# Performance work log

Measured on AMD Instinct MI355X. Metric: run time of the kernel, lower is better.

## Reference

```python
import jax, jax.numpy as jnp
import numpy as np

B, L, E, H = 4, 1024, 2048, 16
DH = E // H
SCALE_BASE = 512.0


def _rotate_every_two(x):
    x1 = x[..., ::2]
    x2 = x[..., 1::2]
    return jnp.stack([-x2, x1], axis=-1).reshape(x.shape)


def _xpos(x, downscale):
    # x: [BH, L, Dh]; non-incremental path => offset = 0
    length = x.shape[1]
    head_dim = x.shape[-1]
    min_pos = -(length // 2)
    positions = jnp.arange(min_pos, length + min_pos, dtype=jnp.float32)  # [L]
    base = (jnp.arange(0, head_dim, 2, dtype=jnp.float32) + 0.4 * head_dim) / (1.4 * head_dim)  # [Dh/2]
    scale = base[None, :] ** (positions[:, None] / SCALE_BASE)  # [L, Dh/2]
    # fixed_pos_embedding over `scale` (seq_len=L, dim=Dh/2), positions 0..L-1
    dim = head_dim // 2
    inv_freq = 1.0 / (10000.0 ** (jnp.arange(0, dim, dtype=jnp.float32) / dim))
    sinusoid = jnp.arange(length, dtype=jnp.float32)[:, None] * inv_freq[None, :]
    sin, cos = jnp.sin(sinusoid), jnp.cos(sinusoid)
    if downscale:
        scale = 1.0 / scale
    sin_s = jnp.repeat(sin * scale, 2, axis=-1)  # duplicate_interleave -> [L, Dh]
    cos_s = jnp.repeat(cos * scale, 2, axis=-1)
    return x * cos_s + _rotate_every_two(x) * sin_s


def setup_inputs() -> dict:
    key = jax.random.key(0)
    ks = jax.random.split(key, 6)
    w_std = 1.0 / np.sqrt(E)
    query = jax.random.normal(ks[0], (B, L, E), dtype=jnp.float32)
    Wq = jax.random.normal(ks[1], (E, E), dtype=jnp.float32) * w_std
    Wk = jax.random.normal(ks[2], (E, E), dtype=jnp.float32) * w_std
    Wv = jax.random.normal(ks[3], (E, E), dtype=jnp.float32) * w_std
    Wo = jax.random.normal(ks[4], (E, E), dtype=jnp.float32) * w_std
    bq = jnp.zeros((E,), jnp.float32)
    bk = jnp.zeros((E,), jnp.float32)
    bv = jnp.zeros((E,), jnp.float32)
    bo = jnp.zeros((E,), jnp.float32)
    # causal additive mask [L, L]: 0 on/below diag, large negative above
    attn_mask = jnp.where(jnp.triu(jnp.ones((L, L), bool), k=1), -1e9, 0.0).astype(jnp.float32)
    rel_pos = jax.random.normal(ks[5], (B * H, L, L), dtype=jnp.float32) * 0.02
    return {"query": query, "Wq": Wq, "bq": bq, "Wk": Wk, "bk": bk, "Wv": Wv,
            "bv": bv, "Wo": Wo, "bo": bo, "attn_mask": attn_mask, "rel_pos": rel_pos}


def reference(query, Wq, bq, Wk, bk, Wv, bv, Wo, bo, attn_mask, rel_pos):
    scaling = DH ** -0.5
    q = (query @ Wq.T + bq) * scaling
    k = query @ Wk.T + bk
    v = query @ Wv.T + bv

    def split(t):  # [B, L, E] -> [B*H, L, Dh]
        return t.reshape(B, L, H, DH).transpose(0, 2, 1, 3).reshape(B * H, L, DH)

    q, k, v = split(q), split(k), split(v)
    k = _xpos(k, downscale=True)
    q = _xpos(q, downscale=False)

    w = jnp.einsum('btd,bsd->bts', q, k)          # [B*H, L, L]
    w = jnp.nan_to_num(w) + attn_mask[None]
    w = w + rel_pos
    w = jax.nn.softmax(w.astype(jnp.float32), axis=-1).astype(w.dtype)
    attn = jnp.einsum('bts,bsd->btd', w, v)       # [B*H, L, Dh]
    attn = attn.reshape(B, H, L, DH).transpose(0, 2, 1, 3).reshape(B, L, E)
    out = attn @ Wo.T + bo
    attn_weights = w.reshape(B, H, L, L).transpose(1, 0, 2, 3)  # [H, B, L, L]
    return out, attn_weights
```

## Files before the change

kernel.cpp:

```cpp
#include <hip/hip_runtime.h>
#include <math.h>

#define BB 4
#define LL 1024
#define EE 2048
#define HH 16
#define DHD 128
#define NTOK 4096
#define NBH 64
#define OUT0_ELEMS 8388608

typedef __attribute__((ext_vector_type(8))) short short8;
typedef __attribute__((ext_vector_type(4))) float f32x4;
typedef __attribute__((ext_vector_type(4))) unsigned short ushort4v;
typedef __attribute__((ext_vector_type(8))) unsigned short ushort8v;

__device__ __forceinline__ unsigned short f2bf(float x) {
    union { float f; unsigned int u; } v; v.f = x;
    unsigned int r = v.u + 0x7FFFu + ((v.u >> 16) & 1u);
    return (unsigned short)(r >> 16);
}
__device__ __forceinline__ float bf2f(unsigned short h) {
    union { unsigned int u; float f; } v; v.u = ((unsigned int)h) << 16;
    return v.f;
}

__device__ __forceinline__ void gload16(const void* g, void* l) {
    __builtin_amdgcn_global_load_lds((const __attribute__((address_space(1))) void*)g,
                                     (__attribute__((address_space(3))) void*)l,
                                     16, 0, 0);
}

__global__ __launch_bounds__(256)
void cvt_all_k(const float* __restrict__ X, const float* __restrict__ Wq,
               const float* __restrict__ Wk, const float* __restrict__ Wv,
               const float* __restrict__ Wo, unsigned short* __restrict__ Xbf,
               unsigned short* __restrict__ Wqkvb, unsigned short* __restrict__ Wob) {
    size_t g = (size_t)(blockIdx.x * 256 + threadIdx.x) * 8;
    if (g >= 25165824u) return;
    const float* src;
    unsigned short* dst;
    if (g < 8388608u) {
        src = X + g; dst = Xbf + g;
    } else {
        size_t rr = g - 8388608u;
        int wi = (int)(rr >> 22);
        size_t o = rr & 4194303u;
        src = (wi == 0 ? Wq : wi == 1 ? Wk : wi == 2 ? Wv : Wo) + o;
        dst = (wi < 3 ? Wqkvb + ((size_t)wi << 22) : Wob) + o;
    }
    float4 a = *(const float4*)(src);
    float4 b = *(const float4*)(src + 4);
    ushort4v u, w;
    u.x = f2bf(a.x); u.y = f2bf(a.y); u.z = f2bf(a.z); u.w = f2bf(a.w);
    w.x = f2bf(b.x); w.y = f2bf(b.y); w.z = f2bf(b.z); w.w = f2bf(b.w);
    *(ushort4v*)(dst) = u;
    *(ushort4v*)(dst + 4) = w;
}

__global__ __launch_bounds__(64) void xpos_table_k(float4* __restrict__ tab) {
    int t = blockIdx.x;
    int j = threadIdx.x;
    float pos = (float)(t - 512);
    float base = (2.0f * (float)j + 51.2f) * (1.0f / 179.2f);
    float sc = powf(base, pos * (1.0f / 512.0f));
    float inv_freq = powf(10000.0f, -(float)j * (1.0f / 64.0f));
    float ang = (float)t * inv_freq;
    float s = sinf(ang);
    float c = cosf(ang);
    tab[(t << 6) | j] = make_float4(c * sc, s * sc, c / sc, s / sc);
}

template <int MODE>
__global__ __launch_bounds__(512, 2)
void mm8_k(const unsigned short* __restrict__ Abf, const unsigned short* __restrict__ Bw,
           const float* __restrict__ bq, const float* __restrict__ bk,
           const float* __restrict__ bv, unsigned short* __restrict__ qb,
           unsigned short* __restrict__ kb, unsigned short* __restrict__ vt,
           const float4* __restrict__ tab, float* __restrict__ Cout,
           float scaling) {
    __shared__ alignas(16) char smem[98304];

    const int tid = threadIdx.x;
    const int lane = tid & 63;
    const int wid = tid >> 6;
    const int wr = wid >> 2;
    const int wcn = wid & 3;
    const int fr = lane & 15, fq = lane >> 4;

    const int m0 = blockIdx.y * 128, n0 = blockIdx.x * 256;

    auto stageA = [&](int T) {
        char* dst = smem + ((T & 1) << 14);
        const unsigned short* src = Abf + (size_t)m0 * 2048 + T * 64;
#pragma unroll
        for (int j = 0; j < 2; ++j) {
            int o = (j * 512 + tid) * 16;
            int r = o >> 7;
            int cs = ((o & 127) >> 4) ^ (r & 7);
            gload16(src + (size_t)r * 2048 + cs * 8, dst + o);
        }
    };
    auto stageB = [&](int T, int half) {
        char* dst = smem + 32768 + ((T & 1) << 15) + (half << 14);
        const unsigned short* src = Bw + (size_t)(n0 + half * 128) * 2048 + T * 64;
#pragma unroll
        for (int j = 0; j < 2; ++j) {
            int o = (j * 512 + tid) * 16;
            int r = o >> 7;
            int cs = ((o & 127) >> 4) ^ (r & 7);
            gload16(src + (size_t)r * 2048 + cs * 8, dst + o);
        }
    };
    auto rdA = [&](int buf, int mi, int ks) -> short8 {
        int rl = (wr << 6) + mi * 16 + fr;
        const char* base = smem + (buf << 14);
        return *(const short8*)(base + rl * 128 + ((ks * 4 + fq) ^ (rl & 7)) * 16);
    };
    auto rdB = [&](int buf, int ni, int ks) -> short8 {
        int rb = wcn * 64 + ni * 16 + fr;
        const char* base = smem + 32768 + (buf << 15) + ((rb >> 7) << 14);
        int rh = rb & 127;
        return *(const short8*)(base + rh * 128 + ((ks * 4 + fq) ^ (rh & 7)) * 16);
    };

    f32x4 acc[4][4];
#pragma unroll
    for (int i = 0; i < 4; ++i)
#pragma unroll
        for (int j = 0; j < 4; ++j) acc[i][j] = (f32x4){0.f, 0.f, 0.f, 0.f};

    stageA(0); stageB(0, 0); stageB(0, 1); stageB(1, 0); stageB(1, 1);

    for (int T = 0; T < 32; ++T) {
        const int buf = T & 1;
        if (T < 31) asm volatile("s_waitcnt vmcnt(4)" ::: "memory");
        else        asm volatile("s_waitcnt vmcnt(0)" ::: "memory");
        __builtin_amdgcn_s_barrier();

        short8 a0[2][2], a1[2][2], b0[2][2], b1[2][2];

#pragma unroll
        for (int mi = 0; mi < 2; ++mi) { a0[mi][0] = rdA(buf, mi, 0); a0[mi][1] = rdA(buf, mi, 1); }
#pragma unroll
        for (int ni = 0; ni < 2; ++ni) { b0[ni][0] = rdB(buf, ni, 0); b0[ni][1] = rdB(buf, ni, 1); }
        if (T < 31) stageA(T + 1);
        __builtin_amdgcn_s_barrier();
        __builtin_amdgcn_s_setprio(1);
#pragma unroll
        for (int mi = 0; mi < 2; ++mi)
#pragma unroll
            for (int ni = 0; ni < 2; ++ni) {
                acc[mi][ni] = __builtin_amdgcn_mfma_f32_16x16x32_bf16(a0[mi][0], b0[ni][0], acc[mi][ni], 0, 0, 0);
                acc[mi][ni] = __builtin_amdgcn_mfma_f32_16x16x32_bf16(a0[mi][1], b0[ni][1], acc[mi][ni], 0, 0, 0);
            }
        __builtin_amdgcn_s_setprio(0);
        __builtin_amdgcn_s_barrier();

#pragma unroll
        for (int ni = 0; ni < 2; ++ni) { b1[ni][0] = rdB(buf, ni + 2, 0); b1[ni][1] = rdB(buf, ni + 2, 1); }
        __builtin_amdgcn_s_barrier();
        __builtin_amdgcn_s_setprio(1);
#pragma unroll
        for (int mi = 0; mi < 2; ++mi)
#pragma unroll
            for (int ni = 0; ni < 2; ++ni) {
                acc[mi][ni + 2] = __builtin_amdgcn_mfma_f32_16x16x32_bf16(a0[mi][0], b1[ni][0], acc[mi][ni + 2], 0, 0, 0);
                acc[mi][ni + 2] = __builtin_amdgcn_mfma_f32_16x16x32_bf16(a0[mi][1], b1[ni][1], acc[mi][ni + 2], 0, 0, 0);
            }
        __builtin_amdgcn_s_setprio(0);
        __builtin_amdgcn_s_barrier();

#pragma unroll
        for (int mi = 0; mi < 2; ++mi) { a1[mi][0] = rdA(buf, mi + 2, 0); a1[mi][1] = rdA(buf, mi + 2, 1); }
        if (T < 30) stageB(T + 2, 0);
        __builtin_amdgcn_s_barrier();
        __builtin_amdgcn_s_setprio(1);
#pragma unroll
        for (int mi = 0; mi < 2; ++mi)
#pragma unroll
            for (int ni = 0; ni < 2; ++ni) {
                acc[mi + 2][ni] = __builtin_amdgcn_mfma_f32_16x16x32_bf16(a1[mi][0], b0[ni][0], acc[mi + 2][ni], 0, 0, 0);
                acc[mi + 2][ni] = __builtin_amdgcn_mfma_f32_16x16x32_bf16(a1[mi][1], b0[ni][1], acc[mi + 2][ni], 0, 0, 0);
            }
        __builtin_amdgcn_s_setprio(0);
        __builtin_amdgcn_s_barrier();

        if (T < 30) stageB(T + 2, 1);
        __builtin_amdgcn_s_barrier();
        __builtin_amdgcn_s_setprio(1);
#pragma unroll
        for (int mi = 0; mi < 2; ++mi)
#pragma unroll
            for (int ni = 0; ni < 2; ++ni) {
                acc[mi + 2][ni + 2] = __builtin_amdgcn_mfma_f32_16x16x32_bf16(a1[mi][0], b1[ni][0], acc[mi + 2][ni + 2], 0, 0, 0);
                acc[mi + 2][ni + 2] = __builtin_amdgcn_mfma_f32_16x16x32_bf16(a1[mi][1], b1[ni][1], acc[mi + 2][ni + 2], 0, 0, 0);
            }
        __builtin_amdgcn_s_setprio(0);
        __builtin_amdgcn_s_barrier();
    }

    if constexpr (MODE == 1) {
        const float* bias = bq;
#pragma unroll
        for (int mi = 0; mi < 4; ++mi)
#pragma unroll
            for (int ni = 0; ni < 4; ++ni)
#pragma unroll
                for (int rg = 0; rg < 4; ++rg) {
                    int m = m0 + wr * 64 + mi * 16 + fq * 4 + rg;
                    int n = n0 + wcn * 64 + ni * 16 + fr;
                    Cout[(size_t)m * EE + n] = acc[mi][ni][rg] + bias[n];
                }
        return;
    } else {
        const int w = n0 >> 11;
        const float* bsel = (w == 0) ? bq : (w == 1) ? bk : bv;
        const float alpha = (w == 0) ? scaling : 1.0f;
        const int hbase = (n0 & 2047) >> 7;
        const int b_ = m0 >> 10;
        const int m0r = m0 & 1023;
        float* slab = (float*)smem;

        unsigned short* qk = (w == 0) ? qb : kb;
        __syncthreads();
#pragma unroll
        for (int sl = 0; sl < 4; ++sl) {
            if (wr == (sl >> 1)) {
#pragma unroll
                for (int mi2 = 0; mi2 < 2; ++mi2) {
                    int mi = ((sl & 1) << 1) + mi2;
#pragma unroll
                    for (int ni = 0; ni < 4; ++ni) {
                        int scol = wcn * 64 + ni * 16 + fr;
                        float bias = bsel[(n0 & 2047) + scol];
#pragma unroll
                        for (int rg = 0; rg < 4; ++rg) {
                            int srow = (mi2 << 4) + fq * 4 + rg;
                            slab[srow * 260 + scol] = alpha * (acc[mi][ni][rg] + bias);
                        }
                    }
                }
            }
            __syncthreads();

            if (w < 2) {
                int sr = tid >> 4, cg = tid & 15;
                int t = m0r + (sl << 5) + sr;
                int h = hbase + (cg >> 3);
                int d0 = (cg & 7) << 4;
                const float* SR = slab + sr * 260 + cg * 16;
                ushort8v h0, h1;
#pragma unroll
                for (int p = 0; p < 4; ++p) {
                    float x = SR[2 * p], y = SR[2 * p + 1];
                    float4 tb = tab[(t << 6) | ((d0 >> 1) + p)];
                    float c = (w == 0) ? tb.x : tb.z;
                    float s = (w == 0) ? tb.y : tb.w;
                    h0[2 * p]     = f2bf(x * c - y * s);
                    h0[2 * p + 1] = f2bf(y * c + x * s);
                }
#pragma unroll
                for (int p = 0; p < 4; ++p) {
                    float x = SR[8 + 2 * p], y = SR[8 + 2 * p + 1];
                    float4 tb = tab[(t << 6) | ((d0 >> 1) + 4 + p)];
                    float c = (w == 0) ? tb.x : tb.z;
                    float s = (w == 0) ? tb.y : tb.w;
                    h1[2 * p]     = f2bf(x * c - y * s);
                    h1[2 * p + 1] = f2bf(y * c + x * s);
                }
                unsigned short* DR = qk + (((size_t)(b_ * HH + h)) << 17) + ((size_t)t << 7) + d0;
                *(ushort8v*)(DR) = h0;
                *(ushort8v*)(DR + 8) = h1;
            } else {
                int vcol = tid >> 1, th = tid & 1;
                int h = hbase + (vcol >> 7), d = vcol & 127;
                ushort8v h0, h1;
#pragma unroll
                for (int p = 0; p < 8; ++p)
                    h0[p] = f2bf(slab[(th * 16 + p) * 260 + vcol]);
#pragma unroll
                for (int p = 0; p < 8; ++p)
                    h1[p] = f2bf(slab[(th * 16 + 8 + p) * 260 + vcol]);
                unsigned short* DR = vt + (((size_t)((b_ * HH + h) * 128 + d)) << 10)
                                     + m0r + (sl << 5) + th * 16;
                *(ushort8v*)(DR) = h0;
                *(ushort8v*)(DR + 8) = h1;
            }
            __syncthreads();
        }
    }
}

__global__ __launch_bounds__(256)
void scores_k(const unsigned short* __restrict__ qb, const unsigned short* __restrict__ kb,
              const float* __restrict__ rel, unsigned short* __restrict__ ebuf,
              float* __restrict__ psum) {
    __shared__ alignas(16) char smem[16384];
    unsigned short* lA = (unsigned short*)smem;
    unsigned short* lB = (unsigned short*)(smem + 8192);
    float* slab = (float*)smem;

    const int tid = threadIdx.x;
    const int lane = tid & 63, wave = tid >> 6;
    const int wr = wave >> 1, wc = wave & 1;
    const int fr = lane & 15, fq = lane >> 4;

    const int flat = blockIdx.y * 36 + blockIdx.x;
    const int xcd = flat & 7, rmp = flat >> 3;
    int idx = rmp % 36;
    const int bh = (rmp / 36) * 8 + xcd;

    int tt = (int)((sqrtf(8.f * (float)idx + 1.f) - 1.f) * 0.5f);
    while ((tt + 1) * (tt + 2) / 2 <= idx) ++tt;
    while (tt * (tt + 1) / 2 > idx) --tt;
    const int ss = idx - tt * (tt + 1) / 2;
    const int t0 = tt << 7, s0 = ss << 7;

    const unsigned short* Q = qb + ((size_t)bh << 17);
    const unsigned short* K = kb + ((size_t)bh << 17);

    f32x4 acc[4][4];
#pragma unroll
    for (int i = 0; i < 4; ++i)
#pragma unroll
        for (int j = 0; j < 4; ++j) acc[i][j] = (f32x4){0.f, 0.f, 0.f, 0.f};

    for (int k0 = 0; k0 < 128; k0 += 32) {
#pragma unroll
        for (int i = 0; i < 2; ++i) {
            int c = i * 256 + tid;
            int r = c >> 2, kc = c & 3;
            gload16(Q + (size_t)(t0 + r) * 128 + k0 + kc * 8, &lA[c * 8]);
        }
#pragma unroll
        for (int i = 0; i < 2; ++i) {
            int c = i * 256 + tid;
            int r = c >> 2, kc = c & 3;
            gload16(K + (size_t)(s0 + r) * 128 + k0 + kc * 8, &lB[c * 8]);
        }
        __syncthreads();

        short8 afr[4], bfr[4];
#pragma unroll
        for (int mi = 0; mi < 4; ++mi)
            afr[mi] = *(const short8*)&lA[(wr * 64 + mi * 16 + fr) * 32 + fq * 8];
#pragma unroll
        for (int ni = 0; ni < 4; ++ni)
            bfr[ni] = *(const short8*)&lB[(wc * 64 + ni * 16 + fr) * 32 + fq * 8];
#pragma unroll
        for (int mi = 0; mi < 4; ++mi)
#pragma unroll
            for (int ni = 0; ni < 4; ++ni)
                acc[mi][ni] = __builtin_amdgcn_mfma_f32_16x16x32_bf16(
                    afr[mi], bfr[ni], acc[mi][ni], 0, 0, 0);
        __syncthreads();
    }

    unsigned short* EO = ebuf + ((size_t)bh << 20);
    const float* RLb = rel + ((size_t)bh << 20);
#pragma unroll
    for (int sl = 0; sl < 4; ++sl) {
        if (wr == (sl >> 1)) {
#pragma unroll
            for (int mi2 = 0; mi2 < 2; ++mi2) {
                int mi = ((sl & 1) << 1) + mi2;
#pragma unroll
                for (int ni = 0; ni < 4; ++ni)
#pragma unroll
                    for (int r = 0; r < 4; ++r) {
                        int srow = (mi2 << 4) + (fq << 2) + r;
                        int col = (wc << 6) + (ni << 4) + fr;
                        slab[srow * 128 + (col ^ (((srow >> 2) & 3) << 4))] = acc[mi][ni][r];
                    }
            }
        }
        __syncthreads();
        {
            int srow = tid >> 3;
            int tg = t0 + (sl << 5) + srow;
            const float* RL = RLb + ((size_t)tg << 10) + s0;
            unsigned short* ER = EO + ((size_t)tg << 10) + s0;
            float rsum = 0.f;
#pragma unroll
            for (int c = 0; c < 4; ++c) {
                int col = ((tid & 7) << 2) + (c << 5);
                float4 sv = *(const float4*)&slab[srow * 128 + (col ^ (((srow >> 2) & 3) << 4))];
                float4 rl = *(const float4*)(RL + col);
                float4 e;
                e.x = (s0 + col     <= tg) ? __expf(sv.x + rl.x - 15.f) : 0.f;
                e.y = (s0 + col + 1 <= tg) ? __expf(sv.y + rl.y - 15.f) : 0.f;
                e.z = (s0 + col + 2 <= tg) ? __expf(sv.z + rl.z - 15.f) : 0.f;
                e.w = (s0 + col + 3 <= tg) ? __expf(sv.w + rl.w - 15.f) : 0.f;
                ushort4v h;
                h.x = f2bf(e.x); h.y = f2bf(e.y); h.z = f2bf(e.z); h.w = f2bf(e.w);
                *(ushort4v*)(ER + col) = h;
                rsum += e.x + e.y + e.z + e.w;
            }
            rsum += __shfl_xor(rsum, 1);
            rsum += __shfl_xor(rsum, 2);
            rsum += __shfl_xor(rsum, 4);
            if ((tid & 7) == 0)
                psum[((((size_t)bh << 10) + tg) << 3) + ss] = rsum;
        }
        __syncthreads();
    }
}

__global__ __launch_bounds__(256)
void pvw_k(const unsigned short* __restrict__ ebuf, const unsigned short* __restrict__ vt,
           const float* __restrict__ psum, float* __restrict__ attnP,
           unsigned short* __restrict__ am) {
    __shared__ alignas(16) unsigned short lE[64 * 64];
    __shared__ alignas(16) unsigned short lV[128 * 64];
    __shared__ float lInvF[64];

    const int tid = threadIdx.x;
    const int lane = tid & 63, wave = tid >> 6;
    const int wr = wave >> 1, wc = wave & 1;
    const int fr = lane & 15, fq = lane >> 4;
    const int strip = 15 - blockIdx.y;
    const int t0 = strip << 6;
    const int bh = blockIdx.x;
    const int hh = bh & 15, bb = bh >> 4;
    const int n_s = (t0 >> 6) + 1;

    const unsigned short* EB = ebuf + ((size_t)bh << 20) + ((size_t)t0 << 10);
    const unsigned short* Vb = vt + ((size_t)bh << 17);
    float* PO = attnP + (((size_t)(hh * BB + bb)) << 20) + ((size_t)t0 << 10);

    if (tid < 64) {
        const float* p = psum + ((((size_t)bh << 10) + t0 + tid) << 3);
        const int tt = t0 >> 7;
        float s = 0.f;
#pragma unroll
        for (int j = 0; j < 8; ++j) s += (j <= tt) ? p[j] : 0.f;
        lInvF[tid] = 1.f / s;
    }
    __syncthreads();

    f32x4 acc[2][4];
#pragma unroll
    for (int i = 0; i < 2; ++i)
#pragma unroll
        for (int j = 0; j < 4; ++j) acc[i][j] = (f32x4){0.f, 0.f, 0.f, 0.f};

    for (int j = 0; j < n_s; ++j) {
        int s0 = j << 6;
#pragma unroll
        for (int i = 0; i < 2; ++i) {
            int o = (i * 256 + tid) * 16;
            int r = o >> 7;
            int cb = (o & 127) ^ ((r & 7) << 4);
            gload16(EB + (size_t)r * 1024 + s0 + (cb >> 1), (char*)lE + o);
        }
#pragma unroll
        for (int i = 0; i < 4; ++i) {
            int o = (i * 256 + tid) * 16;
            int r = o >> 7;
            int cb = (o & 127) ^ ((r & 7) << 4);
            gload16(Vb + (size_t)r * 1024 + s0 + (cb >> 1), (char*)lV + o);
        }
        __syncthreads();

        {
            int row = tid >> 2, col0 = (tid & 3) << 4;
            float inv = lInvF[row];
            float* PR = PO + (size_t)row * 1024 + s0 + col0;
#pragma unroll
            for (int cc = 0; cc < 2; ++cc) {
                int cbyte = ((col0 + cc * 8) * 2) ^ ((row & 7) << 4);
                ushort8v ev = *(const ushort8v*)((const char*)lE + row * 128 + cbyte);
                float4 p0, p1;
                p0.x = bf2f(ev[0]) * inv; p0.y = bf2f(ev[1]) * inv;
                p0.z = bf2f(ev[2]) * inv; p0.w = bf2f(ev[3]) * inv;
                p1.x = bf2f(ev[4]) * inv; p1.y = bf2f(ev[5]) * inv;
                p1.z = bf2f(ev[6]) * inv; p1.w = bf2f(ev[7]) * inv;
                *(float4*)(PR + cc * 8) = p0;
                *(float4*)(PR + cc * 8 + 4) = p1;
            }
        }

#pragma unroll
        for (int ks = 0; ks < 2; ++ks) {
            short8 pf[2], vf[4];
#pragma unroll
            for (int mi = 0; mi < 2; ++mi) {
                int row = wr * 32 + mi * 16 + fr;
                int cb = (ks * 64 + fq * 16) ^ ((row & 7) << 4);
                pf[mi] = *(const short8*)((const char*)lE + row * 128 + cb);
            }
#pragma unroll
            for (int ni = 0; ni < 4; ++ni) {
                int row = wc * 64 + ni * 16 + fr;
                int cb = (ks * 64 + fq * 16) ^ ((row & 7) << 4);
                vf[ni] = *(const short8*)((const char*)lV + row * 128 + cb);
            }
#pragma unroll
            for (int mi = 0; mi < 2; ++mi)
#pragma unroll
                for (int ni = 0; ni < 4; ++ni)
                    acc[mi][ni] = __builtin_amdgcn_mfma_f32_16x16x32_bf16(
                        pf[mi], vf[ni], acc[mi][ni], 0, 0, 0);
        }
        __syncthreads();
    }

    {
        int row = tid >> 2;
        float4 z = make_float4(0.f, 0.f, 0.f, 0.f);
        for (int c = (n_s << 6) + ((tid & 3) << 2); c < 1024; c += 16)
            *(float4*)(PO + (size_t)row * 1024 + c) = z;
    }

#pragma unroll
    for (int mi = 0; mi < 2; ++mi)
#pragma unroll
        for (int ni = 0; ni < 4; ++ni)
#pragma unroll
            for (int r = 0; r < 4; ++r) {
                int tl = wr * 32 + mi * 16 + fq * 4 + r;
                int d = wc * 64 + ni * 16 + fr;
                float o = acc[mi][ni][r] * lInvF[tl];
                am[(((size_t)(bb * 1024 + t0 + tl)) << 11) + hh * 128 + d] = f2bf(o);
            }
}

extern "C" void kernel_launch(void* const* d_in, const int* in_sizes, int n_in,
                              void* d_out, int out_size, void* d_ws, size_t ws_size,
                              hipStream_t stream) {
    const float* query = (const float*)d_in[0];
    const float* Wq    = (const float*)d_in[1];
    const float* bq    = (const float*)d_in[2];
    const float* Wk    = (const float*)d_in[3];
    const float* bk    = (const float*)d_in[4];
    const float* Wv    = (const float*)d_in[5];
    const float* bv    = (const float*)d_in[6];
    const float* Wo    = (const float*)d_in[7];
    const float* bo    = (const float*)d_in[8];
    const float* rel   = (const float*)d_in[10];

    float* out    = (float*)d_out;
    float* attn_w = out + OUT0_ELEMS;

    char* w = (char*)d_ws;
    unsigned short* Xbf   = (unsigned short*)(w);
    unsigned short* Wqkvb = (unsigned short*)(w + (16 << 20));
    unsigned short* Wob   = (unsigned short*)(w + (40 << 20));
    unsigned short* qb    = (unsigned short*)(w + (48 << 20));
    unsigned short* kb    = (unsigned short*)(w + (64 << 20));
    unsigned short* vt    = (unsigned short*)(w + (80 << 20));
    unsigned short* am    = (unsigned short*)(w + (96 << 20));
    float4* tab           = (float4*)(w + (112 << 20));
    float* psum           = (float*)(w + (113u << 20));
    unsigned short* ebuf  = (unsigned short*)(w + (128u << 20));

    const float scaling = 0.08838834764831845f;

    xpos_table_k<<<LL, 64, 0, stream>>>(tab);

    cvt_all_k<<<12288, 256, 0, stream>>>(query, Wq, Wk, Wv, Wo, Xbf, Wqkvb, Wob);

    dim3 gqkv(24, 32);
    mm8_k<0><<<gqkv, 512, 0, stream>>>(Xbf, Wqkvb, bq, bk, bv, qb, kb, vt, tab,
                                       nullptr, scaling);

    dim3 gsc(36, NBH);
    scores_k<<<gsc, 256, 0, stream>>>(qb, kb, rel, ebuf, psum);

    dim3 gpv(NBH, 16);
    pvw_k<<<gpv, 256, 0, stream>>>(ebuf, vt, psum, attn_w, am);

    dim3 gout(8, 32);
    mm8_k<1><<<gout, 512, 0, stream>>>(am, Wob, bo, nullptr, nullptr, nullptr,
                                       nullptr, nullptr, tab, out, 1.0f);
}
```

Baseline: 426.7 us.

## Double-buffer LDS tiles in scores and PV kernels to overlap loads with MFMA

Both the QK^T scores kernel and the PV/weights kernel now keep two LDS buffers and issue the global-to-LDS loads for the next k-step or s-tile before computing the current one. Partial s_waitcnt vmcnt waits and raw s_barrier replace the full __syncthreads, so in-flight prefetches are not drained. The aim is to hide global load latency behind MFMA work. In exchange it doubles LDS use per block, which may lower occupancy, and it relies on hand-counted vmcnt values that must match the number of outstanding loads.

```diff
diff --git a/kernel.cpp b/kernel.cpp
--- a/kernel.cpp
+++ b/kernel.cpp
@@ -296,9 +296,7 @@
 void scores_k(const unsigned short* __restrict__ qb, const unsigned short* __restrict__ kb,
               const float* __restrict__ rel, unsigned short* __restrict__ ebuf,
               float* __restrict__ psum) {
-    __shared__ alignas(16) char smem[16384];
-    unsigned short* lA = (unsigned short*)smem;
-    unsigned short* lB = (unsigned short*)(smem + 8192);
+    __shared__ alignas(16) char smem[32768];
     float* slab = (float*)smem;
 
     const int tid = threadIdx.x;
@@ -320,41 +318,53 @@
     const unsigned short* Q = qb + ((size_t)bh << 17);
     const unsigned short* K = kb + ((size_t)bh << 17);
 
-    f32x4 acc[4][4];
-#pragma unroll
-    for (int i = 0; i < 4; ++i)
-#pragma unroll
-        for (int j = 0; j < 4; ++j) acc[i][j] = (f32x4){0.f, 0.f, 0.f, 0.f};
-
-    for (int k0 = 0; k0 < 128; k0 += 32) {
+    auto stage = [&](int ks) {
+        int b = ks & 1;
+        int k0 = ks << 5;
+        unsigned short* A = (unsigned short*)(smem + b * 8192);
+        unsigned short* Bm = (unsigned short*)(smem + 16384 + b * 8192);
 #pragma unroll
         for (int i = 0; i < 2; ++i) {
             int c = i * 256 + tid;
             int r = c >> 2, kc = c & 3;
-            gload16(Q + (size_t)(t0 + r) * 128 + k0 + kc * 8, &lA[c * 8]);
+            gload16(Q + (size_t)(t0 + r) * 128 + k0 + kc * 8, &A[c * 8]);
         }
 #pragma unroll
         for (int i = 0; i < 2; ++i) {
             int c = i * 256 + tid;
             int r = c >> 2, kc = c & 3;
-            gload16(K + (size_t)(s0 + r) * 128 + k0 + kc * 8, &lB[c * 8]);
-        }
-        __syncthreads();
-
+            gload16(K + (size_t)(s0 + r) * 128 + k0 + kc * 8, &Bm[c * 8]);
+        }
+    };
+
+    f32x4 acc[4][4];
+#pragma unroll
+    for (int i = 0; i < 4; ++i)
+#pragma unroll
+        for (int j = 0; j < 4; ++j) acc[i][j] = (f32x4){0.f, 0.f, 0.f, 0.f};
+
+    stage(0);
+    for (int ks = 0; ks < 4; ++ks) {
+        if (ks < 3) { stage(ks + 1); asm volatile("s_waitcnt vmcnt(4)" ::: "memory"); }
+        else        { asm volatile("s_waitcnt vmcnt(0)" ::: "memory"); }
+        __builtin_amdgcn_s_barrier();
+
+        const unsigned short* A = (const unsigned short*)(smem + (ks & 1) * 8192);
+        const unsigned short* Bm = (const unsigned short*)(smem + 16384 + (ks & 1) * 8192);
         short8 afr[4], bfr[4];
 #pragma unroll
         for (int mi = 0; mi < 4; ++mi)
-            afr[mi] = *(const short8*)&lA[(wr * 64 + mi * 16 + fr) * 32 + fq * 8];
+            afr[mi] = *(const short8*)&A[(wr * 64 + mi * 16 + fr) * 32 + fq * 8];
 #pragma unroll
         for (int ni = 0; ni < 4; ++ni)
-            bfr[ni] = *(const short8*)&lB[(wc * 64 + ni * 16 + fr) * 32 + fq * 8];
+            bfr[ni] = *(const short8*)&Bm[(wc * 64 + ni * 16 + fr) * 32 + fq * 8];
 #pragma unroll
         for (int mi = 0; mi < 4; ++mi)
 #pragma unroll
             for (int ni = 0; ni < 4; ++ni)
                 acc[mi][ni] = __builtin_amdgcn_mfma_f32_16x16x32_bf16(
                     afr[mi], bfr[ni], acc[mi][ni], 0, 0, 0);
-        __syncthreads();
+        __builtin_amdgcn_s_barrier();
     }
 
     unsigned short* EO = ebuf + ((size_t)bh << 20);
@@ -411,8 +421,8 @@
 void pvw_k(const unsigned short* __restrict__ ebuf, const unsigned short* __restrict__ vt,
            const float* __restrict__ psum, float* __restrict__ attnP,
            unsigned short* __restrict__ am) {
-    __shared__ alignas(16) unsigned short lE[64 * 64];
-    __shared__ alignas(16) unsigned short lV[128 * 64];
+    __shared__ alignas(16) unsigned short lE[2][64 * 64];
+    __shared__ alignas(16) unsigned short lV[2][128 * 64];
     __shared__ float lInvF[64];
 
     const int tid = threadIdx.x;
@@ -423,7 +433,7 @@
     const int t0 = strip << 6;
     const int bh = blockIdx.x;
     const int hh = bh & 15, bb = bh >> 4;
-    const int n_s = (t0 >> 6) + 1;
+    const int n_s = strip + 1;
 
     const unsigned short* EB = ebuf + ((size_t)bh << 20) + ((size_t)t0 << 10);
     const unsigned short* Vb = vt + ((size_t)bh << 17);
@@ -439,29 +449,38 @@
     }
     __syncthreads();
 
-    f32x4 acc[2][4];
-#pragma unroll
-    for (int i = 0; i < 2; ++i)
-#pragma unroll
-        for (int j = 0; j < 4; ++j) acc[i][j] = (f32x4){0.f, 0.f, 0.f, 0.f};
-
-    for (int j = 0; j < n_s; ++j) {
+    auto stage = [&](int j) {
+        int b = j & 1;
         int s0 = j << 6;
 #pragma unroll
         for (int i = 0; i < 2; ++i) {
             int o = (i * 256 + tid) * 16;
             int r = o >> 7;
             int cb = (o & 127) ^ ((r & 7) << 4);
-            gload16(EB + (size_t)r * 1024 + s0 + (cb >> 1), (char*)lE + o);
+            gload16(EB + (size_t)r * 1024 + s0 + (cb >> 1), (char*)lE[b] + o);
         }
 #pragma unroll
         for (int i = 0; i < 4; ++i) {
             int o = (i * 256 + tid) * 16;
             int r = o >> 7;
             int cb = (o & 127) ^ ((r & 7) << 4);
-            gload16(Vb + (size_t)r * 1024 + s0 + (cb >> 1), (char*)lV + o);
-        }
-        __syncthreads();
+            gload16(Vb + (size_t)r * 1024 + s0 + (cb >> 1), (char*)lV[b] + o);
+        }
+    };
+
+    f32x4 acc[2][4];
+#pragma unroll
+    for (int i = 0; i < 2; ++i)
+#pragma unroll
+        for (int j = 0; j < 4; ++j) acc[i][j] = (f32x4){0.f, 0.f, 0.f, 0.f};
+
+    stage(0);
+    for (int j = 0; j < n_s; ++j) {
+        const int b = j & 1;
+        if (j + 1 < n_s) { stage(j + 1); asm volatile("s_waitcnt vmcnt(6)" ::: "memory"); }
+        else             { asm volatile("s_waitcnt vmcnt(0)" ::: "memory"); }
+        __builtin_amdgcn_s_barrier();
+        const int s0 = j << 6;
 
         {
             int row = tid >> 2, col0 = (tid & 3) << 4;
@@ -470,7 +489,7 @@
 #pragma unroll
             for (int cc = 0; cc < 2; ++cc) {
                 int cbyte = ((col0 + cc * 8) * 2) ^ ((row & 7) << 4);
-                ushort8v ev = *(const ushort8v*)((const char*)lE + row * 128 + cbyte);
+                ushort8v ev = *(const ushort8v*)((const char*)lE[b] + row * 128 + cbyte);
                 float4 p0, p1;
                 p0.x = bf2f(ev[0]) * inv; p0.y = bf2f(ev[1]) * inv;
                 p0.z = bf2f(ev[2]) * inv; p0.w = bf2f(ev[3]) * inv;
@@ -488,13 +507,13 @@
             for (int mi = 0; mi < 2; ++mi) {
                 int row = wr * 32 + mi * 16 + fr;
                 int cb = (ks * 64 + fq * 16) ^ ((row & 7) << 4);
-                pf[mi] = *(const short8*)((const char*)lE + row * 128 + cb);
+                pf[mi] = *(const short8*)((const char*)lE[b] + row * 128 + cb);
             }
 #pragma unroll
             for (int ni = 0; ni < 4; ++ni) {
                 int row = wc * 64 + ni * 16 + fr;
                 int cb = (ks * 64 + fq * 16) ^ ((row & 7) << 4);
-                vf[ni] = *(const short8*)((const char*)lV + row * 128 + cb);
+                vf[ni] = *(const short8*)((const char*)lV[b] + row * 128 + cb);
             }
 #pragma unroll
             for (int mi = 0; mi < 2; ++mi)
@@ -503,7 +522,7 @@
                     acc[mi][ni] = __builtin_amdgcn_mfma_f32_16x16x32_bf16(
                         pf[mi], vf[ni], acc[mi][ni], 0, 0, 0);
         }
-        __syncthreads();
+        __builtin_amdgcn_s_barrier();
     }
 
     {
```

Result: slower. 436.7 us (+2.4%).

## Split normalized attention-weight write out of PV kernel into streaming kernel

Applied to the files above, without the earlier changes.

Removes the fp32 normalized-probability store and the zero-fill of masked columns from the PV matmul kernel, leaving it as a pure bf16 PV product. A new row-per-wave kernel re-reads the unnormalized bf16 exponentials and the partial sums, normalizes them and writes the full attention-weight matrix, including zeros. The aim is to stop the large, causally imbalanced store traffic from stalling the MFMA loop, and to let the store run as a uniform streaming pass. The cost is an extra kernel launch and a second read of the exponential buffer.

```diff
diff --git a/kernel.cpp b/kernel.cpp
--- a/kernel.cpp
+++ b/kernel.cpp
@@ -408,9 +408,8 @@
 }
 
 __global__ __launch_bounds__(256)
-void pvw_k(const unsigned short* __restrict__ ebuf, const unsigned short* __restrict__ vt,
-           const float* __restrict__ psum, float* __restrict__ attnP,
-           unsigned short* __restrict__ am) {
+void pv_k(const unsigned short* __restrict__ ebuf, const unsigned short* __restrict__ vt,
+          const float* __restrict__ psum, unsigned short* __restrict__ am) {
     __shared__ alignas(16) unsigned short lE[64 * 64];
     __shared__ alignas(16) unsigned short lV[128 * 64];
     __shared__ float lInvF[64];
@@ -423,11 +422,10 @@
     const int t0 = strip << 6;
     const int bh = blockIdx.x;
     const int hh = bh & 15, bb = bh >> 4;
-    const int n_s = (t0 >> 6) + 1;
+    const int n_s = strip + 1;
 
     const unsigned short* EB = ebuf + ((size_t)bh << 20) + ((size_t)t0 << 10);
     const unsigned short* Vb = vt + ((size_t)bh << 17);
-    float* PO = attnP + (((size_t)(hh * BB + bb)) << 20) + ((size_t)t0 << 10);
 
     if (tid < 64) {
         const float* p = psum + ((((size_t)bh << 10) + t0 + tid) << 3);
@@ -437,7 +435,6 @@
         for (int j = 0; j < 8; ++j) s += (j <= tt) ? p[j] : 0.f;
         lInvF[tid] = 1.f / s;
     }
-    __syncthreads();
 
     f32x4 acc[2][4];
 #pragma unroll
@@ -447,6 +444,7 @@
 
     for (int j = 0; j < n_s; ++j) {
         int s0 = j << 6;
+        __syncthreads();
 #pragma unroll
         for (int i = 0; i < 2; ++i) {
             int o = (i * 256 + tid) * 16;
@@ -463,24 +461,6 @@
         }
         __syncthreads();
 
-        {
-            int row = tid >> 2, col0 = (tid & 3) << 4;
-            float inv = lInvF[row];
-            float* PR = PO + (size_t)row * 1024 + s0 + col0;
-#pragma unroll
-            for (int cc = 0; cc < 2; ++cc) {
-                int cbyte = ((col0 + cc * 8) * 2) ^ ((row & 7) << 4);
-                ushort8v ev = *(const ushort8v*)((const char*)lE + row * 128 + cbyte);
-                float4 p0, p1;
-                p0.x = bf2f(ev[0]) * inv; p0.y = bf2f(ev[1]) * inv;
-                p0.z = bf2f(ev[2]) * inv; p0.w = bf2f(ev[3]) * inv;
-                p1.x = bf2f(ev[4]) * inv; p1.y = bf2f(ev[5]) * inv;
-                p1.z = bf2f(ev[6]) * inv; p1.w = bf2f(ev[7]) * inv;
-                *(float4*)(PR + cc * 8) = p0;
-                *(float4*)(PR + cc * 8 + 4) = p1;
-            }
-        }
-
 #pragma unroll
         for (int ks = 0; ks < 2; ++ks) {
             short8 pf[2], vf[4];
@@ -503,14 +483,6 @@
                     acc[mi][ni] = __builtin_amdgcn_mfma_f32_16x16x32_bf16(
                         pf[mi], vf[ni], acc[mi][ni], 0, 0, 0);
         }
-        __syncthreads();
-    }
-
-    {
-        int row = tid >> 2;
-        float4 z = make_float4(0.f, 0.f, 0.f, 0.f);
-        for (int c = (n_s << 6) + ((tid & 3) << 2); c < 1024; c += 16)
-            *(float4*)(PO + (size_t)row * 1024 + c) = z;
     }
 
 #pragma unroll
@@ -524,6 +496,51 @@
                 float o = acc[mi][ni][r] * lInvF[tl];
                 am[(((size_t)(bb * 1024 + t0 + tl)) << 11) + hh * 128 + d] = f2bf(o);
             }
+}
+
+__global__ __launch_bounds__(256)
+void normP_k(const unsigned short* __restrict__ ebuf, const float* __restrict__ psum,
+             float* __restrict__ attnP) {
+    const int gid = blockIdx.x * 4 + (threadIdx.x >> 6);
+    const int lane = threadIdx.x & 63;
+    const int bh = gid >> 10, t = gid & 1023;
+    const int hh = bh & 15, bb = bh >> 4;
+    const int tt = t >> 7;
+    const int kend = (tt + 1) << 7;
+
+    const float* p = psum + ((size_t)gid << 3);
+    float s = 0.f;
+#pragma unroll
+    for (int j = 0; j < 8; ++j) s += (j <= tt) ? p[j] : 0.f;
+    const float inv = 1.f / s;
+
+    const unsigned short* ER = ebuf + ((size_t)gid << 10);
+    float* PR = attnP + (((size_t)(hh * BB + bb)) << 20) + ((size_t)t << 10);
+    const int col = lane << 4;
+
+    if (col < kend) {
+        ushort8v e0 = *(const ushort8v*)(ER + col);
+        ushort8v e1 = *(const ushort8v*)(ER + col + 8);
+        float4 o0, o1, o2, o3;
+        o0.x = bf2f(e0[0]) * inv; o0.y = bf2f(e0[1]) * inv;
+        o0.z = bf2f(e0[2]) * inv; o0.w = bf2f(e0[3]) * inv;
+        o1.x = bf2f(e0[4]) * inv; o1.y = bf2f(e0[5]) * inv;
+        o1.z = bf2f(e0[6]) * inv; o1.w = bf2f(e0[7]) * inv;
+        o2.x = bf2f(e1[0]) * inv; o2.y = bf2f(e1[1]) * inv;
+        o2.z = bf2f(e1[2]) * inv; o2.w = bf2f(e1[3]) * inv;
+        o3.x = bf2f(e1[4]) * inv; o3.y = bf2f(e1[5]) * inv;
+        o3.z = bf2f(e1[6]) * inv; o3.w = bf2f(e1[7]) * inv;
+        *(float4*)(PR + col)      = o0;
+        *(float4*)(PR + col + 4)  = o1;
+        *(float4*)(PR + col + 8)  = o2;
+        *(float4*)(PR + col + 12) = o3;
+    } else {
+        float4 z = make_float4(0.f, 0.f, 0.f, 0.f);
+        *(float4*)(PR + col)      = z;
+        *(float4*)(PR + col + 4)  = z;
+        *(float4*)(PR + col + 8)  = z;
+        *(float4*)(PR + col + 12) = z;
+    }
 }
 
 extern "C" void kernel_launch(void* const* d_in, const int* in_sizes, int n_in,
@@ -569,7 +586,9 @@
     scores_k<<<gsc, 256, 0, stream>>>(qb, kb, rel, ebuf, psum);
 
     dim3 gpv(NBH, 16);
-    pvw_k<<<gpv, 256, 0, stream>>>(ebuf, vt, psum, attn_w, am);
+    pv_k<<<gpv, 256, 0, stream>>>(ebuf, vt, psum, am);
+
+    normP_k<<<16384, 256, 0, stream>>>(ebuf, psum, attn_w);
 
     dim3 gout(8, 32);
     mm8_k<1><<<gout, 512, 0, stream>>>(am, Wob, bo, nullptr, nullptr, nullptr,
```

After: 420.3 us. No clear change (-1.5%).
